# Optimization experiments

Measured on AMD Instinct MI355X. Metric: run time of the kernel, lower is better.

The kernel has to match this reference:

```python
import jax, jax.numpy as jnp
import numpy as np

D_MODEL = 1024

def setup_inputs() -> dict:
    key = jax.random.key(0)
    ks = jax.random.split(key, 7)
    s = 1.0 / np.sqrt(D_MODEL)
    x = jax.random.normal(ks[0], (4, 2048, D_MODEL), dtype=jnp.float32)
    wq_w = jax.random.uniform(ks[1], (D_MODEL, D_MODEL), jnp.float32, -s, s)
    wq_b = jax.random.uniform(ks[2], (D_MODEL,), jnp.float32, -s, s)
    wk_w = jax.random.uniform(ks[3], (D_MODEL, D_MODEL), jnp.float32, -s, s)
    wk_b = jax.random.uniform(ks[4], (D_MODEL,), jnp.float32, -s, s)
    wv_w = jax.random.uniform(ks[5], (D_MODEL, D_MODEL), jnp.float32, -s, s)
    wv_b = jax.random.uniform(ks[6], (D_MODEL,), jnp.float32, -s, s)
    return {"x": x, "wq_w": wq_w, "wq_b": wq_b, "wk_w": wk_w, "wk_b": wk_b, "wv_w": wv_w, "wv_b": wv_b}

def reference(x, wq_w, wq_b, wk_w, wk_b, wv_w, wv_b):
    # Linear: x @ W^T + b (torch nn.Linear convention)
    q = jnp.einsum('bsd,ed->bse', x, wq_w) + wq_b
    k = jnp.einsum('bsd,ed->bse', x, wk_w) + wk_b
    v = jnp.einsum('bsd,ed->bse', x, wv_w) + wv_b
    scale = 1.0 / jnp.sqrt(jnp.asarray(k.shape[-1], dtype=q.dtype))
    logits = jnp.einsum('bqd,bkd->bqk', q, k) * scale  # [B, S, S]
    attn = jax.nn.softmax(logits, axis=-1)
    out = jnp.einsum('bqk,bkd->bqd', attn, v)
    return (attn, out)
```

## Files before the change

kernel.cpp:

```cpp
#include <hip/hip_runtime.h>

typedef unsigned short u16;
typedef u16 u16x4 __attribute__((ext_vector_type(4)));
typedef u16 u16x8 __attribute__((ext_vector_type(8)));
typedef __bf16 bf16x8 __attribute__((ext_vector_type(8)));
typedef float f32x4 __attribute__((ext_vector_type(4)));
typedef float f32x16 __attribute__((ext_vector_type(16)));

static __device__ __forceinline__ u16 f2bf(float f) {
  unsigned u = __builtin_bit_cast(unsigned, f);
  u += 0x7fffu + ((u >> 16) & 1u);
  return (u16)(u >> 16);
}
static __device__ __forceinline__ float bf2f(u16 h) {
  return __builtin_bit_cast(float, ((unsigned)h) << 16);
}

static __device__ __forceinline__ void gload_lds16(const u16* g, u16* l) {
  u16* gn = const_cast<u16*>(g);
  __builtin_amdgcn_global_load_lds(
      (__attribute__((address_space(1))) unsigned int*)gn,
      (__attribute__((address_space(3))) unsigned int*)l,
      16, 0, 0);
}

__global__ __launch_bounds__(256)
void cvt_f32_bf16(const float* __restrict__ in, u16* __restrict__ out) {
  const int i = blockIdx.x * 256 + threadIdx.x;
  float4 f = ((const float4*)in)[i];
  u16x4 o = { f2bf(f.x), f2bf(f.y), f2bf(f.z), f2bf(f.w) };
  ((u16x4*)out)[i] = o;
}

__global__ __launch_bounds__(256)
void cvt_w3(const float* __restrict__ a, const float* __restrict__ b,
            const float* __restrict__ c, u16* __restrict__ out) {
  const int blk = blockIdx.x;
  const int w = blk >> 10;
  const float* src = (w == 0) ? a : (w == 1) ? b : c;
  const int i = (blk & 1023) * 256 + threadIdx.x;
  float4 f = ((const float4*)src)[i];
  u16x4 o = { f2bf(f.x), f2bf(f.y), f2bf(f.z), f2bf(f.w) };
  ((u16x4*)(out + (size_t)w * 1048576ULL))[i] = o;
}


#define MM16(a, b, c) __builtin_amdgcn_mfma_f32_16x16x32_bf16(a, b, c, 0, 0, 0)
#define WAITV4 asm volatile("s_waitcnt vmcnt(4)" ::: "memory")
#define WAITNONE (void)0

#define STAGE_A(BUF, J, KT) \
  gload_lds16(Ag + (size_t)(J) * 32 * lda + (KT), AsW + (BUF) * 16384 + (J) * 2048)
#define STAGE_B(BUF, KS, RH, KT) \
  gload_lds16(Bg + (size_t)(RH) * 32 * ldb + (KS) * 32 + (KT), \
              BsW + (BUF) * 16384 + (KS) * 2048 + (RH) * 1024)

#define APTR(BUF, MI, KS) \
  ((const bf16x8*)(ArdBase + (BUF) * 16384 + (MI) * 1024 + ((pA0 ^ ((KS) << 2)) << 3)))
#define BPTR(BUF, NI, KS) \
  ((const bf16x8*)(BrdBase + (BUF) * 16384 + (KS) * 2048 + (NI) * 512))

#define PHASE(BUF, MH, KS, WAITSTMT, ...) do {                              \
    bf16x8 a0 = *APTR(BUF, (MH) * 4 + 0, KS);                               \
    bf16x8 a1 = *APTR(BUF, (MH) * 4 + 1, KS);                               \
    bf16x8 a2 = *APTR(BUF, (MH) * 4 + 2, KS);                               \
    bf16x8 a3 = *APTR(BUF, (MH) * 4 + 3, KS);                               \
    bf16x8 q0 = *BPTR(BUF, 0, KS);                                          \
    bf16x8 q1 = *BPTR(BUF, 1, KS);                                          \
    bf16x8 q2 = *BPTR(BUF, 2, KS);                                          \
    bf16x8 q3 = *BPTR(BUF, 3, KS);                                          \
    __VA_ARGS__;                                                            \
    __builtin_amdgcn_sched_barrier(0);                                      \
    __builtin_amdgcn_s_barrier();                                           \
    __builtin_amdgcn_s_setprio(1);                                          \
    acc[(MH)*4+0][0] = MM16(a0, q0, acc[(MH)*4+0][0]);                      \
    acc[(MH)*4+1][0] = MM16(a1, q0, acc[(MH)*4+1][0]);                      \
    acc[(MH)*4+2][0] = MM16(a2, q0, acc[(MH)*4+2][0]);                      \
    acc[(MH)*4+3][0] = MM16(a3, q0, acc[(MH)*4+3][0]);                      \
    acc[(MH)*4+0][1] = MM16(a0, q1, acc[(MH)*4+0][1]);                      \
    acc[(MH)*4+1][1] = MM16(a1, q1, acc[(MH)*4+1][1]);                      \
    acc[(MH)*4+2][1] = MM16(a2, q1, acc[(MH)*4+2][1]);                      \
    acc[(MH)*4+3][1] = MM16(a3, q1, acc[(MH)*4+3][1]);                      \
    acc[(MH)*4+0][2] = MM16(a0, q2, acc[(MH)*4+0][2]);                      \
    acc[(MH)*4+1][2] = MM16(a1, q2, acc[(MH)*4+1][2]);                      \
    acc[(MH)*4+2][2] = MM16(a2, q2, acc[(MH)*4+2][2]);                      \
    acc[(MH)*4+3][2] = MM16(a3, q2, acc[(MH)*4+3][2]);                      \
    acc[(MH)*4+0][3] = MM16(a0, q3, acc[(MH)*4+0][3]);                      \
    acc[(MH)*4+1][3] = MM16(a1, q3, acc[(MH)*4+1][3]);                      \
    acc[(MH)*4+2][3] = MM16(a2, q3, acc[(MH)*4+2][3]);                      \
    acc[(MH)*4+3][3] = MM16(a3, q3, acc[(MH)*4+3][3]);                      \
    __builtin_amdgcn_s_setprio(0);                                          \
    WAITSTMT;                                                               \
    __builtin_amdgcn_sched_barrier(0);                                      \
    __builtin_amdgcn_s_barrier();                                           \
  } while (0)

template<int MODE>
__global__ __launch_bounds__(512, 2)
void gemm8p(const u16* __restrict__ Ain, const u16* __restrict__ Bin,
            void* __restrict__ Cv,
            const float* __restrict__ b0, const float* __restrict__ b1,
            const float* __restrict__ b2,
            int lda, int ldb, int ldc, int K,
            unsigned long long sA, unsigned long long sB, unsigned long long sC,
            int nbx, int nby)
{
  __shared__ alignas(16) u16 As[2 * 2 * 128 * 64];
  __shared__ alignas(16) u16 Bs[2 * 4 * 2 * 64 * 32];

  const int nbxy = nbx * nby;
  const int bid  = blockIdx.x;
  const int flat = (bid & 7) * ((int)gridDim.x >> 3) + (bid >> 3);
  const int z    = flat / nbxy;
  const int rr   = flat - z * nbxy;
  const int width = nbx << 3;
  const int gid  = rr / width;
  const int rw   = rr - gid * width;
  const int by   = (gid << 3) + (rw & 7);
  const int bx   = rw >> 3;

  const u16* A = Ain + z * sA;
  const u16* B = Bin + z * sB;

  const int tid  = threadIdx.x;
  const int wave = tid >> 6;
  const int lane = tid & 63;
  const int wr   = wave >> 2;
  const int wc   = wave & 3;
  const int l16  = lane & 15;
  const int l4   = lane >> 4;

  const int m0 = by << 8;
  const int n0 = bx << 8;

  const int asr = wc * 8 + (lane >> 3);
  const int asc = ((lane & 7) ^ (lane >> 3)) << 3;
  const u16* Ag = A + (size_t)(m0 + wr * 128 + asr) * lda + asc;
  u16* AsW = As + wr * 8192 + wc * 512;

  const int bsr = wr * 16 + (lane >> 2);
  const int bsc = ((lane & 3) ^ ((lane >> 3) & 3)) << 3;
  const u16* Bg = B + (size_t)(n0 + wc * 64 + bsr) * ldb + bsc;
  u16* BsW = Bs + wc * 4096 + wr * 512;

  const u16* ArdBase = As + (wr * 128 + l16) * 64;
  const int pA0 = l4 ^ (l16 & 7);
  const u16* BrdBase = Bs + wc * 4096 + l16 * 32 + ((l4 ^ ((l16 >> 1) & 3)) << 3);

  f32x4 acc[8][4];
  #pragma unroll
  for (int i = 0; i < 8; ++i)
    #pragma unroll
    for (int j = 0; j < 4; ++j)
      #pragma unroll
      for (int r = 0; r < 4; ++r)
        acc[i][j][r] = 0.f;

  STAGE_A(0, 0, 0); STAGE_A(0, 1, 0);
  STAGE_B(0, 0, 0, 0); STAGE_B(0, 0, 1, 0);
  STAGE_B(0, 1, 0, 0); STAGE_B(0, 1, 1, 0);
  STAGE_A(0, 2, 0); STAGE_A(0, 3, 0);
  WAITV4;
  __builtin_amdgcn_sched_barrier(0);
  __builtin_amdgcn_s_barrier();

  const int NT = K >> 6;
  for (int t = 0; t < NT; t += 2) {
    {
      const int kn = (t + 1) * 64;
      PHASE(0, 0, 0, WAITV4,   STAGE_A(1, 0, kn); STAGE_A(1, 1, kn));
      PHASE(0, 0, 1, WAITV4,   STAGE_B(1, 0, 0, kn); STAGE_B(1, 0, 1, kn));
      PHASE(0, 1, 0, WAITNONE, STAGE_B(1, 1, 0, kn); STAGE_B(1, 1, 1, kn));
      PHASE(0, 1, 1, WAITV4,   STAGE_A(1, 2, kn); STAGE_A(1, 3, kn));
    }
    {
      const int kn = (t + 2 < NT) ? (t + 2) * 64 : 0;
      PHASE(1, 0, 0, WAITV4,   STAGE_A(0, 0, kn); STAGE_A(0, 1, kn));
      PHASE(1, 0, 1, WAITV4,   STAGE_B(0, 0, 0, kn); STAGE_B(0, 0, 1, kn));
      PHASE(1, 1, 0, WAITNONE, STAGE_B(0, 1, 0, kn); STAGE_B(0, 1, 1, kn));
      PHASE(1, 1, 1, WAITV4,   STAGE_A(0, 2, kn); STAGE_A(0, 3, kn));
    }
  }
  asm volatile("s_waitcnt vmcnt(0)" ::: "memory");

  if constexpr (MODE == 0) {
    const int g = n0 >> 10;
    const int colb = (n0 + wc * 64) & 1023;
    const int rowb = m0 + wr * 128 + l4 * 4;
    if (g < 2) {
      u16* Cb = (u16*)Cv + (size_t)g * 8388608ULL;
      const float* bp = (g == 0) ? b0 : b1;
      const float qs = (g == 0) ? 0.03125f : 1.0f;
      #pragma unroll
      for (int ni = 0; ni < 4; ++ni) {
        const int col = colb + ni * 16 + l16;
        const float bv = bp[col];
        #pragma unroll
        for (int mi = 0; mi < 8; ++mi) {
          const int row = rowb + mi * 16;
          #pragma unroll
          for (int r = 0; r < 4; ++r)
            Cb[(size_t)(row + r) * 1024 + col] = f2bf((acc[mi][ni][r] + bv) * qs);
        }
      }
    } else {
      u16* Vt = (u16*)Cv + 16777216ULL;
      #pragma unroll
      for (int ni = 0; ni < 4; ++ni) {
        const int col = colb + ni * 16 + l16;
        const float bv = b2[col];
        #pragma unroll
        for (int mi = 0; mi < 8; ++mi) {
          const int row = rowb + mi * 16;
          u16x4 o;
          #pragma unroll
          for (int r = 0; r < 4; ++r) o[r] = f2bf(acc[mi][ni][r] + bv);
          const size_t idx = ((size_t)((row >> 11) * 1024 + col)) * 2048 + (row & 2047);
          *(u16x4*)&Vt[idx] = o;
        }
      }
    }
  } else {
    u16* Cb = (u16*)Cv + (size_t)z * sC;
    #pragma unroll
    for (int ni = 0; ni < 4; ++ni) {
      const int col = n0 + wc * 64 + ni * 16 + l16;
      #pragma unroll
      for (int mi = 0; mi < 8; ++mi) {
        const int row = m0 + wr * 128 + mi * 16 + l4 * 4;
        #pragma unroll
        for (int r = 0; r < 4; ++r)
          Cb[(size_t)(row + r) * ldc + col] = f2bf(acc[mi][ni][r]);
      }
    }
  }
}

template<int MODE>
__global__ __launch_bounds__(256)
void gemm_bt(const u16* __restrict__ Ain, const u16* __restrict__ Bin,
             void* __restrict__ Cv,
             const float* __restrict__ b0, const float* __restrict__ b1,
             const float* __restrict__ b2,
             int lda, int ldb, int ldc, int K,
             unsigned long long sA, unsigned long long sB, unsigned long long sC,
             int nbx, int nby)
{
  constexpr int BM = 128, BN = 128, BK = 64;
  __shared__ alignas(16) u16 As[BM * BK];
  __shared__ alignas(16) u16 Bs[BN * BK];

  const int nbxy = nbx * nby;
  const int bid  = blockIdx.x;
  const int flat = (bid & 7) * ((int)gridDim.x >> 3) + (bid >> 3);
  const int z    = flat / nbxy;
  const int rr   = flat - z * nbxy;
  const int width = nbx << 3;
  const int gid  = rr / width;
  const int rw   = rr - gid * width;
  const int by   = (gid << 3) + (rw & 7);
  const int bx   = rw >> 3;

  const u16* A = Ain + z * sA;
  const u16* B = Bin + z * sB;

  const int tid  = threadIdx.x;
  const int wave = tid >> 6;
  const int lane = tid & 63;
  const int l32  = lane & 31;
  const int half = lane >> 5;
  const int wr   = wave >> 1;
  const int wc   = wave & 1;

  const int m0 = by * BM;
  const int n0 = bx * BN;

  const int lr = lane >> 3;
  const int sc = ((lane & 7) ^ lr) * 8;
  const u16* Ag = A + (size_t)(m0 + wave * 32 + lr) * lda + sc;
  const u16* Bg = B + (size_t)(n0 + wave * 32 + lr) * ldb + sc;
  u16* Asb = &As[(wave * 32) * BK];
  u16* Bsb = &Bs[(wave * 32) * BK];

  f32x16 acc[2][2];
  #pragma unroll
  for (int i = 0; i < 2; ++i)
    #pragma unroll
    for (int j = 0; j < 2; ++j)
      #pragma unroll
      for (int r = 0; r < 16; ++r)
        acc[i][j][r] = 0.f;

  for (int k0 = 0; k0 < K; k0 += BK) {
    gload_lds16(Ag + k0,                    Asb);
    gload_lds16(Ag + (size_t) 8 * lda + k0, Asb +  8 * BK);
    gload_lds16(Ag + (size_t)16 * lda + k0, Asb + 16 * BK);
    gload_lds16(Ag + (size_t)24 * lda + k0, Asb + 24 * BK);
    gload_lds16(Bg + k0,                    Bsb);
    gload_lds16(Bg + (size_t) 8 * ldb + k0, Bsb +  8 * BK);
    gload_lds16(Bg + (size_t)16 * ldb + k0, Bsb + 16 * BK);
    gload_lds16(Bg + (size_t)24 * ldb + k0, Bsb + 24 * BK);
    __syncthreads();

    #pragma unroll
    for (int ks = 0; ks < 4; ++ks) {
      bf16x8 af[2], bfr[2];
      #pragma unroll
      for (int ti = 0; ti < 2; ++ti) {
        const int row = wr * 64 + ti * 32 + l32;
        const int ch  = ((ks * 2 + half) ^ (row & 7)) * 8;
        af[ti] = *(const bf16x8*)&As[row * BK + ch];
      }
      #pragma unroll
      for (int tj = 0; tj < 2; ++tj) {
        const int row = wc * 64 + tj * 32 + l32;
        const int ch  = ((ks * 2 + half) ^ (row & 7)) * 8;
        bfr[tj] = *(const bf16x8*)&Bs[row * BK + ch];
      }
      #pragma unroll
      for (int ti = 0; ti < 2; ++ti)
        #pragma unroll
        for (int tj = 0; tj < 2; ++tj)
          acc[ti][tj] = __builtin_amdgcn_mfma_f32_32x32x16_bf16(af[ti], bfr[tj], acc[ti][tj], 0, 0, 0);
    }
    __syncthreads();
  }

  const int colb = n0 + wc * 64 + l32;
  const int rowb = m0 + wr * 64 + 4 * half;

  if constexpr (MODE == 3) {
    float* Cf = (float*)Cv + z * sC;
    #pragma unroll
    for (int tj = 0; tj < 2; ++tj) {
      const int col = colb + tj * 32;
      #pragma unroll
      for (int ti = 0; ti < 2; ++ti)
        #pragma unroll
        for (int g4 = 0; g4 < 4; ++g4)
          #pragma unroll
          for (int r = 0; r < 4; ++r) {
            const int row = rowb + ti * 32 + g4 * 8 + r;
            Cf[(size_t)row * ldc + col] = acc[ti][tj][g4 * 4 + r];
          }
    }
  }
}

__global__ __launch_bounds__(256)
void softmax_rows(u16* __restrict__ logits, float* __restrict__ attn) {
  const int row = blockIdx.x;
  const int tid = threadIdx.x;
  u16*   lp = logits + (size_t)row * 2048 + tid * 8;
  float* ap = attn   + (size_t)row * 2048 + tid * 8;

  u16x8 raw = *(const u16x8*)lp;
  float v[8];
  #pragma unroll
  for (int j = 0; j < 8; ++j) v[j] = bf2f(raw[j]);

  float mx = v[0];
  #pragma unroll
  for (int j = 1; j < 8; ++j) mx = fmaxf(mx, v[j]);
  #pragma unroll
  for (int o = 32; o > 0; o >>= 1) mx = fmaxf(mx, __shfl_xor(mx, o, 64));

  __shared__ float smax[4], ssum[4];
  const int wv = tid >> 6, ln = tid & 63;
  if (ln == 0) smax[wv] = mx;
  __syncthreads();
  mx = fmaxf(fmaxf(smax[0], smax[1]), fmaxf(smax[2], smax[3]));

  float s = 0.f;
  #pragma unroll
  for (int j = 0; j < 8; ++j) { v[j] = __expf(v[j] - mx); s += v[j]; }
  #pragma unroll
  for (int o = 32; o > 0; o >>= 1) s += __shfl_xor(s, o, 64);
  if (ln == 0) ssum[wv] = s;
  __syncthreads();
  s = (ssum[0] + ssum[1]) + (ssum[2] + ssum[3]);
  const float inv = 1.f / s;

  u16x8 ob;
  #pragma unroll
  for (int j = 0; j < 8; ++j) { v[j] *= inv; ob[j] = f2bf(v[j]); }
  float4* apv = (float4*)ap;
  apv[0] = make_float4(v[0], v[1], v[2], v[3]);
  apv[1] = make_float4(v[4], v[5], v[6], v[7]);
  *(u16x8*)lp = ob;
}

extern "C" void kernel_launch(void* const* d_in, const int* in_sizes, int n_in,
                              void* d_out, int out_size, void* d_ws, size_t ws_size,
                              hipStream_t stream) {
  (void)in_sizes; (void)n_in; (void)out_size; (void)ws_size;
  const float* x    = (const float*)d_in[0];
  const float* wq_w = (const float*)d_in[1];
  const float* wq_b = (const float*)d_in[2];
  const float* wk_w = (const float*)d_in[3];
  const float* wk_b = (const float*)d_in[4];
  const float* wv_w = (const float*)d_in[5];
  const float* wv_b = (const float*)d_in[6];

  float* attn = (float*)d_out;
  float* outp = attn + 16777216ULL;

  u16* xb   = (u16*)d_ws;
  u16* wcat = xb   + 8388608ULL;
  u16* Qb   = wcat + 3145728ULL;
  u16* Kb   = Qb   + 8388608ULL;
  u16* Vt   = Kb   + 8388608ULL;
  u16* Lg   = Vt   + 8388608ULL;

  cvt_f32_bf16<<<8192, 256, 0, stream>>>(x, xb);
  cvt_w3<<<3072, 256, 0, stream>>>(wq_w, wk_w, wv_w, wcat);

  gemm8p<0><<<384, 512, 0, stream>>>(xb, wcat, Qb, wq_b, wk_b, wv_b,
                                     1024, 1024, 1024, 1024, 0, 0, 0, 12, 32);

  gemm8p<2><<<256, 512, 0, stream>>>(Qb, Kb, Lg, nullptr, nullptr, nullptr,
                                     1024, 1024, 2048, 1024,
                                     2097152ULL, 2097152ULL, 4194304ULL, 8, 8);

  softmax_rows<<<8192, 256, 0, stream>>>(Lg, attn);

  gemm_bt<3><<<512, 256, 0, stream>>>(Lg, Vt, outp, nullptr, nullptr, nullptr,
                                      2048, 2048, 1024, 2048,
                                      4194304ULL, 2097152ULL, 2097152ULL, 8, 16);
}
```

Baseline: 326.4 us.

## Double-buffer LDS fragment reads in registers across GEMM phases

Restructures the GEMM main loop so the LDS fragment reads for the next phase are issued before the current phase's MFMAs run, using two alternating register sets (x/y). Each phase now waits for those reads with lgkmcnt(8) and uses a uniform vmcnt(2) wait instead of the previous mix of vmcnt(4) and no wait. The aim is to hide LDS read latency behind matrix-core work. It costs extra VGPRs for the second fragment set, which could hurt occupancy under launch_bounds(512,2), and the changed wait counts make the correctness of the cross-phase buffer ordering more delicate.

```diff
diff --git a/kernel.cpp b/kernel.cpp
--- a/kernel.cpp
+++ b/kernel.cpp
@@ -46,8 +46,6 @@
 
 
 #define MM16(a, b, c) __builtin_amdgcn_mfma_f32_16x16x32_bf16(a, b, c, 0, 0, 0)
-#define WAITV4 asm volatile("s_waitcnt vmcnt(4)" ::: "memory")
-#define WAITNONE (void)0
 
 #define STAGE_A(BUF, J, KT) \
   gload_lds16(Ag + (size_t)(J) * 32 * lda + (KT), AsW + (BUF) * 16384 + (J) * 2048)
@@ -60,37 +58,41 @@
 #define BPTR(BUF, NI, KS) \
   ((const bf16x8*)(BrdBase + (BUF) * 16384 + (KS) * 2048 + (NI) * 512))
 
-#define PHASE(BUF, MH, KS, WAITSTMT, ...) do {                              \
-    bf16x8 a0 = *APTR(BUF, (MH) * 4 + 0, KS);                               \
-    bf16x8 a1 = *APTR(BUF, (MH) * 4 + 1, KS);                               \
-    bf16x8 a2 = *APTR(BUF, (MH) * 4 + 2, KS);                               \
-    bf16x8 a3 = *APTR(BUF, (MH) * 4 + 3, KS);                               \
-    bf16x8 q0 = *BPTR(BUF, 0, KS);                                          \
-    bf16x8 q1 = *BPTR(BUF, 1, KS);                                          \
-    bf16x8 q2 = *BPTR(BUF, 2, KS);                                          \
-    bf16x8 q3 = *BPTR(BUF, 3, KS);                                          \
-    __VA_ARGS__;                                                            \
+#define RD8(S, BUF, MH, KS) \
+    S##A0 = *APTR(BUF, (MH) * 4 + 0, KS); \
+    S##A1 = *APTR(BUF, (MH) * 4 + 1, KS); \
+    S##A2 = *APTR(BUF, (MH) * 4 + 2, KS); \
+    S##A3 = *APTR(BUF, (MH) * 4 + 3, KS); \
+    S##B0 = *BPTR(BUF, 0, KS); \
+    S##B1 = *BPTR(BUF, 1, KS); \
+    S##B2 = *BPTR(BUF, 2, KS); \
+    S##B3 = *BPTR(BUF, 3, KS)
+
+#define PH(CUR, NXT, MH, NBUF, NMH, NKS, STG) do {                          \
+    RD8(NXT, NBUF, NMH, NKS);                                               \
+    STG;                                                                    \
+    __builtin_amdgcn_s_barrier();                                           \
+    asm volatile("s_waitcnt lgkmcnt(8)" ::: "memory");                      \
     __builtin_amdgcn_sched_barrier(0);                                      \
-    __builtin_amdgcn_s_barrier();                                           \
     __builtin_amdgcn_s_setprio(1);                                          \
-    acc[(MH)*4+0][0] = MM16(a0, q0, acc[(MH)*4+0][0]);                      \
-    acc[(MH)*4+1][0] = MM16(a1, q0, acc[(MH)*4+1][0]);                      \
-    acc[(MH)*4+2][0] = MM16(a2, q0, acc[(MH)*4+2][0]);                      \
-    acc[(MH)*4+3][0] = MM16(a3, q0, acc[(MH)*4+3][0]);                      \
-    acc[(MH)*4+0][1] = MM16(a0, q1, acc[(MH)*4+0][1]);                      \
-    acc[(MH)*4+1][1] = MM16(a1, q1, acc[(MH)*4+1][1]);                      \
-    acc[(MH)*4+2][1] = MM16(a2, q1, acc[(MH)*4+2][1]);                      \
-    acc[(MH)*4+3][1] = MM16(a3, q1, acc[(MH)*4+3][1]);                      \
-    acc[(MH)*4+0][2] = MM16(a0, q2, acc[(MH)*4+0][2]);                      \
-    acc[(MH)*4+1][2] = MM16(a1, q2, acc[(MH)*4+1][2]);                      \
-    acc[(MH)*4+2][2] = MM16(a2, q2, acc[(MH)*4+2][2]);                      \
-    acc[(MH)*4+3][2] = MM16(a3, q2, acc[(MH)*4+3][2]);                      \
-    acc[(MH)*4+0][3] = MM16(a0, q3, acc[(MH)*4+0][3]);                      \
-    acc[(MH)*4+1][3] = MM16(a1, q3, acc[(MH)*4+1][3]);                      \
-    acc[(MH)*4+2][3] = MM16(a2, q3, acc[(MH)*4+2][3]);                      \
-    acc[(MH)*4+3][3] = MM16(a3, q3, acc[(MH)*4+3][3]);                      \
+    acc[(MH)*4+0][0] = MM16(CUR##A0, CUR##B0, acc[(MH)*4+0][0]);            \
+    acc[(MH)*4+1][0] = MM16(CUR##A1, CUR##B0, acc[(MH)*4+1][0]);            \
+    acc[(MH)*4+2][0] = MM16(CUR##A2, CUR##B0, acc[(MH)*4+2][0]);            \
+    acc[(MH)*4+3][0] = MM16(CUR##A3, CUR##B0, acc[(MH)*4+3][0]);            \
+    acc[(MH)*4+0][1] = MM16(CUR##A0, CUR##B1, acc[(MH)*4+0][1]);            \
+    acc[(MH)*4+1][1] = MM16(CUR##A1, CUR##B1, acc[(MH)*4+1][1]);            \
+    acc[(MH)*4+2][1] = MM16(CUR##A2, CUR##B1, acc[(MH)*4+2][1]);            \
+    acc[(MH)*4+3][1] = MM16(CUR##A3, CUR##B1, acc[(MH)*4+3][1]);            \
+    acc[(MH)*4+0][2] = MM16(CUR##A0, CUR##B2, acc[(MH)*4+0][2]);            \
+    acc[(MH)*4+1][2] = MM16(CUR##A1, CUR##B2, acc[(MH)*4+1][2]);            \
+    acc[(MH)*4+2][2] = MM16(CUR##A2, CUR##B2, acc[(MH)*4+2][2]);            \
+    acc[(MH)*4+3][2] = MM16(CUR##A3, CUR##B2, acc[(MH)*4+3][2]);            \
+    acc[(MH)*4+0][3] = MM16(CUR##A0, CUR##B3, acc[(MH)*4+0][3]);            \
+    acc[(MH)*4+1][3] = MM16(CUR##A1, CUR##B3, acc[(MH)*4+1][3]);            \
+    acc[(MH)*4+2][3] = MM16(CUR##A2, CUR##B3, acc[(MH)*4+2][3]);            \
+    acc[(MH)*4+3][3] = MM16(CUR##A3, CUR##B3, acc[(MH)*4+3][3]);            \
     __builtin_amdgcn_s_setprio(0);                                          \
-    WAITSTMT;                                                               \
+    asm volatile("s_waitcnt vmcnt(2)" ::: "memory");                        \
     __builtin_amdgcn_sched_barrier(0);                                      \
     __builtin_amdgcn_s_barrier();                                           \
   } while (0)
@@ -156,30 +158,30 @@
       for (int r = 0; r < 4; ++r)
         acc[i][j][r] = 0.f;
 
+  bf16x8 xA0, xA1, xA2, xA3, xB0, xB1, xB2, xB3;
+  bf16x8 yA0, yA1, yA2, yA3, yB0, yB1, yB2, yB3;
+
   STAGE_A(0, 0, 0); STAGE_A(0, 1, 0);
   STAGE_B(0, 0, 0, 0); STAGE_B(0, 0, 1, 0);
   STAGE_B(0, 1, 0, 0); STAGE_B(0, 1, 1, 0);
   STAGE_A(0, 2, 0); STAGE_A(0, 3, 0);
-  WAITV4;
+  asm volatile("s_waitcnt vmcnt(0)" ::: "memory");
   __builtin_amdgcn_sched_barrier(0);
   __builtin_amdgcn_s_barrier();
+  RD8(x, 0, 0, 0);
 
   const int NT = K >> 6;
   for (int t = 0; t < NT; t += 2) {
-    {
-      const int kn = (t + 1) * 64;
-      PHASE(0, 0, 0, WAITV4,   STAGE_A(1, 0, kn); STAGE_A(1, 1, kn));
-      PHASE(0, 0, 1, WAITV4,   STAGE_B(1, 0, 0, kn); STAGE_B(1, 0, 1, kn));
-      PHASE(0, 1, 0, WAITNONE, STAGE_B(1, 1, 0, kn); STAGE_B(1, 1, 1, kn));
-      PHASE(0, 1, 1, WAITV4,   STAGE_A(1, 2, kn); STAGE_A(1, 3, kn));
-    }
-    {
-      const int kn = (t + 2 < NT) ? (t + 2) * 64 : 0;
-      PHASE(1, 0, 0, WAITV4,   STAGE_A(0, 0, kn); STAGE_A(0, 1, kn));
-      PHASE(1, 0, 1, WAITV4,   STAGE_B(0, 0, 0, kn); STAGE_B(0, 0, 1, kn));
-      PHASE(1, 1, 0, WAITNONE, STAGE_B(0, 1, 0, kn); STAGE_B(0, 1, 1, kn));
-      PHASE(1, 1, 1, WAITV4,   STAGE_A(0, 2, kn); STAGE_A(0, 3, kn));
-    }
+    const int k1 = (t + 1) * 64;
+    const int k2 = (t + 2 < NT) ? (t + 2) * 64 : 0;
+    PH(x, y, 0, 0, 0, 1, STAGE_A(1, 0, k1); STAGE_A(1, 1, k1));
+    PH(y, x, 0, 0, 1, 0, STAGE_B(1, 0, 0, k1); STAGE_B(1, 0, 1, k1));
+    PH(x, y, 1, 0, 1, 1, STAGE_B(1, 1, 0, k1); STAGE_B(1, 1, 1, k1));
+    PH(y, x, 1, 1, 0, 0, STAGE_A(1, 2, k1); STAGE_A(1, 3, k1));
+    PH(x, y, 0, 1, 0, 1, STAGE_A(0, 0, k2); STAGE_A(0, 1, k2));
+    PH(y, x, 0, 1, 1, 0, STAGE_B(0, 0, 0, k2); STAGE_B(0, 0, 1, k2));
+    PH(x, y, 1, 1, 1, 1, STAGE_B(0, 1, 0, k2); STAGE_B(0, 1, 1, k2));
+    PH(y, x, 1, 0, 0, 0, STAGE_A(0, 2, k2); STAGE_A(0, 3, k2));
   }
   asm volatile("s_waitcnt vmcnt(0)" ::: "memory");
 
```

Result: no change. 332.0 us (+1.7%).
